# Kernel tuning notes

Hardware: AMD Instinct MI355X
Metric: run time of the kernel (lower is better)

Reference implementation:

```python
import jax, jax.numpy as jnp
import numpy as np

B, F, R, C = 16384, 256, 32, 16
H1, H2 = 128, 32        # FS-MLP hidden sizes
G1, G2 = 256, 64        # consequent MLP hidden sizes


def setup_inputs() -> dict:
    key = jax.random.key(0)
    ks = jax.random.split(key, 16)
    s = 0.05
    return {
        "data": jax.random.normal(ks[0], (B, F), jnp.float32),
        # per-rule antecedent params (torch inits proto=0, var=1; randomize proto for a nontrivial test)
        "proto": jax.random.normal(ks[1], (R, F), jnp.float32) * 0.1,
        "var": jnp.full((R, F), 0.05, jnp.float32),
        # shared FS-MLP: Linear(F,128)->ReLU->Linear(128,32)->ReLU->Linear(32,1)->ReLU
        "Wf1": jax.random.normal(ks[2], (H1, F), jnp.float32) * s,
        "bf1": jax.random.normal(ks[3], (H1,), jnp.float32) * s,
        "Wf2": jax.random.normal(ks[4], (H2, H1), jnp.float32) * s,
        "bf2": jax.random.normal(ks[5], (H2,), jnp.float32) * s,
        "Wf3": jax.random.normal(ks[6], (1, H2), jnp.float32) * s,
        "bf3": jax.random.normal(ks[7], (1,), jnp.float32) * s,
        # per-rule consequent MLP (stacked over rule dim): Linear(F,256)->ELU->Linear(256,64)->ELU->Linear(64,C)
        "Wc1": jax.random.normal(ks[8], (R, G1, F), jnp.float32) * s,
        "bc1": jax.random.normal(ks[9], (R, G1), jnp.float32) * s,
        "Wc2": jax.random.normal(ks[10], (R, G2, G1), jnp.float32) * s,
        "bc2": jax.random.normal(ks[11], (R, G2), jnp.float32) * s,
        "Wc3": jax.random.normal(ks[12], (R, C, G2), jnp.float32) * s,
        "bc3": jax.random.normal(ks[13], (R, C), jnp.float32) * s,
    }


def reference(data, proto, var, Wf1, bf1, Wf2, bf2, Wf3, bf3,
              Wc1, bc1, Wc2, bc2, Wc3, bc3):
    # Antecedent: Gaussian membership per rule -> [R, B, F]
    v = jnp.clip(var, 1e-4, 0.1)
    mem = jnp.exp(-(data[None, :, :] - proto[:, None, :]) ** 2
                  / (2.0 * v[:, None, :] ** 2))
    # Shared firing-strength MLP on each rule's membership tensor -> [R, B]
    h = jax.nn.relu(jnp.einsum('rbf,of->rbo', mem, Wf1) + bf1)
    h = jax.nn.relu(jnp.einsum('rbo,po->rbp', h, Wf2) + bf2)
    fs_ini = jax.nn.relu(jnp.einsum('rbp,qp->rbq', h, Wf3) + bf3)[..., 0]
    fire_strength = jax.nn.softmax(fs_ini.T, axis=1)  # [B, R], softmax over rules
    # Per-rule consequent MLPs on raw data (batched over rule dim) -> [R, B, C]
    c = jax.nn.elu(jnp.einsum('bf,rhf->rbh', data, Wc1) + bc1[:, None, :])
    c = jax.nn.elu(jnp.einsum('rbh,rgh->rbg', c, Wc2) + bc2[:, None, :])
    c = jax.nn.relu(jnp.einsum('rbg,rcg->rbc', c, Wc3) + bc3[:, None, :])
    # Softmax-weighted sum over rules -> [B, C]
    outputs = jnp.einsum('rbc,br->bc', c, fire_strength)
    return outputs, fire_strength
```

## Files before the change

### kernel.cpp

```cpp
#include <hip/hip_runtime.h>
#include <hip/hip_bf16.h>

#define BN 16384
#define FN 256
#define RN 32
#define CN 16
#define H1N 128
#define H2N 32
#define G1N 256
#define G2N 64

typedef __bf16 bf16_t;
typedef __bf16 bf16x8 __attribute__((ext_vector_type(8)));
typedef __bf16 bf16x4 __attribute__((ext_vector_type(4)));
typedef float f32x4 __attribute__((ext_vector_type(4)));

#define OFF_DATA   0UL
#define OFF_WF1    8388608UL
#define OFF_WF2    8454144UL
#define OFF_WC1    8462336UL
#define OFF_WC2    12656640UL
#define OFF_WC3    13705216UL
#define OFF_FSINI  13770752UL
#define OFF_C3     15867904UL

__device__ __forceinline__ f32x4 mfma16(bf16x8 a, bf16x8 b, f32x4 c) {
  return __builtin_amdgcn_mfma_f32_16x16x32_bf16(a, b, c, 0, 0, 0);
}

__device__ __forceinline__ float elu_f(float v) {
  float e = __builtin_amdgcn_exp2f(v * 1.44269504f) - 1.0f;
  return v > 0.f ? v : e;
}

__device__ __forceinline__ bf16x8 lfrag(const char* base, int strideB, int n0, int k0, int lane) {
  int row = n0 + (lane & 15);
  int off = (k0 * 2 + ((lane >> 4) << 4)) ^ ((row & 7) << 4);
  return *(const bf16x8*)(base + row * strideB + off);
}

__device__ __forceinline__ void pack_frag8(const float* __restrict__ src, bf16_t* __restrict__ dst,
                                           int NT, int KS, int g) {
  int per = NT * KS * 64;
  int r = g / per;
  int local = g - r * per;
  int lane = local & 63;
  int fr = local >> 6;
  int ks = fr / NT;
  int nt = fr - ks * NT;
  int N = NT * 16, K = KS * 32;
  int n = nt * 16 + (lane & 15);
  int k = ks * 32 + ((lane >> 4) << 3);
  const float* s = src + (long)r * N * K + (long)n * K + k;
  float4 a = *(const float4*)s;
  float4 b = *(const float4*)(s + 4);
  bf16x8 o;
  o[0] = (bf16_t)a.x; o[1] = (bf16_t)a.y; o[2] = (bf16_t)a.z; o[3] = (bf16_t)a.w;
  o[4] = (bf16_t)b.x; o[5] = (bf16_t)b.y; o[6] = (bf16_t)b.z; o[7] = (bf16_t)b.w;
  *(bf16x8*)(dst + (long)g * 8) = o;
}

#define G_DATA 524288
#define G_WC1  262144
#define G_WC2  65536
#define G_WF1  4096
#define G_WC3  4096
#define G_WF2  512
#define G_TOTAL (G_DATA + G_WC1 + G_WC2 + G_WF1 + G_WC3 + G_WF2)

__global__ __launch_bounds__(256) void k0_pack(
    const float* __restrict__ data, const float* __restrict__ Wf1, const float* __restrict__ Wf2,
    const float* __restrict__ Wc1, const float* __restrict__ Wc2, const float* __restrict__ Wc3,
    char* __restrict__ ws)
{
  int g = blockIdx.x * 256 + threadIdx.x;
  if (g < G_DATA) {
    const float* s = data + (long)g * 8;
    float4 a = *(const float4*)s, b = *(const float4*)(s + 4);
    bf16x8 o;
    o[0] = (bf16_t)a.x; o[1] = (bf16_t)a.y; o[2] = (bf16_t)a.z; o[3] = (bf16_t)a.w;
    o[4] = (bf16_t)b.x; o[5] = (bf16_t)b.y; o[6] = (bf16_t)b.z; o[7] = (bf16_t)b.w;
    *(bf16x8*)((bf16_t*)(ws + OFF_DATA) + (long)g * 8) = o;
    return;
  }
  g -= G_DATA;
  if (g < G_WC1) { pack_frag8(Wc1, (bf16_t*)(ws + OFF_WC1), 16, 8, g); return; }
  g -= G_WC1;
  if (g < G_WC2) { pack_frag8(Wc2, (bf16_t*)(ws + OFF_WC2), 4, 8, g); return; }
  g -= G_WC2;
  if (g < G_WF1) { pack_frag8(Wf1, (bf16_t*)(ws + OFF_WF1), 8, 8, g); return; }
  g -= G_WF1;
  if (g < G_WC3) { pack_frag8(Wc3, (bf16_t*)(ws + OFF_WC3), 1, 2, g); return; }
  g -= G_WF2 + G_WC3 - G_WC3;
  if (g < G_WC3) { }
  g -= 0;
  {
    if (g >= G_WC3) { g -= G_WC3; }
    if (g < G_WF2) { pack_frag8(Wf2, (bf16_t*)(ws + OFF_WF2), 2, 4, g); return; }
  }
}

__global__ __launch_bounds__(512, 4) void k1_fs(
    const float* __restrict__ data, const float* __restrict__ proto, const float* __restrict__ var,
    const float* __restrict__ bf1g, const float* __restrict__ bf2g,
    const float* __restrict__ Wf3g, const float* __restrict__ bf3g,
    const bf16_t* __restrict__ Wf1p, const bf16_t* __restrict__ Wf2p,
    float* __restrict__ fsini)
{
  __shared__ float proto_s[FN];
  __shared__ float ivar_s[FN];
  __shared__ __attribute__((aligned(16))) char mem_lds[128 * 512];

  const int r   = blockIdx.x >> 7;
  const int b0  = (blockIdx.x & 127) << 7;
  const int tid = threadIdx.x;
  const int lane = tid & 63;
  const int w   = tid >> 6;

  if (tid < FN) {
    proto_s[tid] = proto[r * FN + tid];
    float v = var[r * FN + tid];
    v = fminf(fmaxf(v, 1e-4f), 0.1f);
    ivar_s[tid] = 1.4426950408889634f * 0.5f / (v * v);
  }
  __syncthreads();

  {
    const int row = tid >> 2;
    const int f0  = (tid & 3) << 6;
    const float* dp = data + (long)(b0 + row) * FN + f0;
    char* mrow = mem_lds + row * 512;
    const int sw = (row & 7) << 4;
    #pragma unroll
    for (int i = 0; i < 8; ++i) {
      const int f = f0 + i * 8;
      float4 x0 = *(const float4*)(dp + i * 8);
      float4 x1 = *(const float4*)(dp + i * 8 + 4);
      bf16x8 m; float d;
      d = x0.x - proto_s[f + 0]; m[0] = (bf16_t)__builtin_amdgcn_exp2f(-d * d * ivar_s[f + 0]);
      d = x0.y - proto_s[f + 1]; m[1] = (bf16_t)__builtin_amdgcn_exp2f(-d * d * ivar_s[f + 1]);
      d = x0.z - proto_s[f + 2]; m[2] = (bf16_t)__builtin_amdgcn_exp2f(-d * d * ivar_s[f + 2]);
      d = x0.w - proto_s[f + 3]; m[3] = (bf16_t)__builtin_amdgcn_exp2f(-d * d * ivar_s[f + 3]);
      d = x1.x - proto_s[f + 4]; m[4] = (bf16_t)__builtin_amdgcn_exp2f(-d * d * ivar_s[f + 4]);
      d = x1.y - proto_s[f + 5]; m[5] = (bf16_t)__builtin_amdgcn_exp2f(-d * d * ivar_s[f + 5]);
      d = x1.z - proto_s[f + 6]; m[6] = (bf16_t)__builtin_amdgcn_exp2f(-d * d * ivar_s[f + 6]);
      d = x1.w - proto_s[f + 7]; m[7] = (bf16_t)__builtin_amdgcn_exp2f(-d * d * ivar_s[f + 7]);
      *(bf16x8*)(mrow + ((f * 2) ^ sw)) = m;
    }
  }
  __syncthreads();

  const int wm = w >> 2;
  const int wn = w & 3;
  f32x4 acc[4][2] = {};
  #pragma unroll
  for (int ks = 0; ks < 8; ++ks) {
    bf16x8 a[4], bb[2];
    #pragma unroll
    for (int i = 0; i < 4; ++i)
      a[i] = *(const bf16x8*)(Wf1p + (((ks * 8 + wm * 4 + i) * 64 + lane)) * 8);
    #pragma unroll
    for (int j = 0; j < 2; ++j)
      bb[j] = lfrag(mem_lds, 512, wn * 32 + j * 16, ks * 32, lane);
    #pragma unroll
    for (int i = 0; i < 4; ++i)
      #pragma unroll
      for (int j = 0; j < 2; ++j)
        acc[i][j] = mfma16(a[i], bb[j], acc[i][j]);
  }
  __syncthreads();

  #pragma unroll
  for (int i = 0; i < 4; ++i) {
    const int hb = wm * 64 + i * 16 + ((lane >> 4) << 2);
    f32x4 bias = *(const f32x4*)(bf1g + hb);
    #pragma unroll
    for (int j = 0; j < 2; ++j) {
      const int b = wn * 32 + j * 16 + (lane & 15);
      bf16x4 o;
      #pragma unroll
      for (int q = 0; q < 4; ++q)
        o[q] = (bf16_t)fmaxf(acc[i][j][q] + bias[q], 0.f);
      *(bf16x4*)(mem_lds + b * 256 + ((hb * 2) ^ ((b & 7) << 4))) = o;
    }
  }
  __syncthreads();

  float* h2s = (float*)(mem_lds + 32768);
  const int mt = w >> 2;
  f32x4 acc2[2] = {};
  #pragma unroll
  for (int ks = 0; ks < 4; ++ks) {
    bf16x8 a = *(const bf16x8*)(Wf2p + (((ks * 2 + mt) * 64 + lane)) * 8);
    #pragma unroll
    for (int j = 0; j < 2; ++j) {
      bf16x8 bb = lfrag(mem_lds, 256, (w & 3) * 32 + j * 16, ks * 32, lane);
      acc2[j] = mfma16(a, bb, acc2[j]);
    }
  }
  {
    const int p0 = mt * 16 + ((lane >> 4) << 2);
    f32x4 bias = *(const f32x4*)(bf2g + p0);
    #pragma unroll
    for (int j = 0; j < 2; ++j) {
      const int b = (w & 3) * 32 + j * 16 + (lane & 15);
      f32x4 o;
      #pragma unroll
      for (int q = 0; q < 4; ++q) o[q] = fmaxf(acc2[j][q] + bias[q], 0.f);
      *(f32x4*)(h2s + b * 40 + p0) = o;
    }
  }
  __syncthreads();

  if (tid < 128) {
    float s = bf3g[0];
    const float* hrow = h2s + tid * 40;
    #pragma unroll
    for (int p = 0; p < H2N; ++p) s += hrow[p] * Wf3g[p];
    fsini[(long)(b0 + tid) * RN + r] = fmaxf(s, 0.f);
  }
}

__global__ __launch_bounds__(256) void k2_softmax(const float* __restrict__ fsini,
                                                  float* __restrict__ fire)
{
  int b = blockIdx.x * 256 + threadIdx.x;
  float v[RN];
  const float4* p = (const float4*)(fsini + (long)b * RN);
  #pragma unroll
  for (int i = 0; i < RN / 4; ++i) {
    float4 t = p[i];
    v[4 * i] = t.x; v[4 * i + 1] = t.y; v[4 * i + 2] = t.z; v[4 * i + 3] = t.w;
  }
  float m = v[0];
  #pragma unroll
  for (int i = 1; i < RN; ++i) m = fmaxf(m, v[i]);
  float s = 0.f;
  #pragma unroll
  for (int i = 0; i < RN; ++i) { v[i] = expf(v[i] - m); s += v[i]; }
  float inv = 1.f / s;
  float4* o = (float4*)(fire + (long)b * RN);
  #pragma unroll
  for (int i = 0; i < RN / 4; ++i) {
    float4 t; t.x = v[4 * i] * inv; t.y = v[4 * i + 1] * inv;
    t.z = v[4 * i + 2] * inv; t.w = v[4 * i + 3] * inv;
    o[i] = t;
  }
}

__global__ __launch_bounds__(512, 4) void k3_cons(
    const bf16_t* __restrict__ datab,
    const bf16_t* __restrict__ Wc1p, const bf16_t* __restrict__ Wc2p, const bf16_t* __restrict__ Wc3p,
    const float* __restrict__ bc1, const float* __restrict__ bc2, const float* __restrict__ bc3,
    float* __restrict__ c3buf)
{
  __shared__ __attribute__((aligned(16))) char a_lds[128 * 512];
  __shared__ __attribute__((aligned(16))) char c2_lds[128 * 128];

  const int r   = blockIdx.x >> 7;
  const int b0  = (blockIdx.x & 127) << 7;
  const int tid = threadIdx.x;
  const int lane = tid & 63;
  const int w   = tid >> 6;

  {
    const int row = tid >> 2;
    const int e0  = (tid & 3) << 6;
    const bf16_t* sp = datab + (long)(b0 + row) * FN + e0;
    char* drow = a_lds + row * 512;
    const int sw = (row & 7) << 4;
    #pragma unroll
    for (int i = 0; i < 8; ++i) {
      bf16x8 v = *(const bf16x8*)(sp + i * 8);
      *(bf16x8*)(drow + (((e0 + i * 8) * 2) ^ sw)) = v;
    }
  }
  __syncthreads();

  const int wm = w >> 1;
  const int wn = w & 1;
  const bf16_t* W1 = Wc1p + (long)r * G1N * FN;
  f32x4 acc[4][4] = {};
  #pragma unroll
  for (int ks = 0; ks < 8; ++ks) {
    bf16x8 a[4], bb[4];
    #pragma unroll
    for (int i = 0; i < 4; ++i)
      a[i] = *(const bf16x8*)(W1 + (((ks * 16 + wm * 4 + i) * 64 + lane)) * 8);
    #pragma unroll
    for (int j = 0; j < 4; ++j)
      bb[j] = lfrag(a_lds, 512, wn * 64 + j * 16, ks * 32, lane);
    #pragma unroll
    for (int i = 0; i < 4; ++i)
      #pragma unroll
      for (int j = 0; j < 4; ++j)
        acc[i][j] = mfma16(a[i], bb[j], acc[i][j]);
  }
  __syncthreads();

  #pragma unroll
  for (int i = 0; i < 4; ++i) {
    const int g1b = wm * 64 + i * 16 + ((lane >> 4) << 2);
    f32x4 bias = *(const f32x4*)(bc1 + r * G1N + g1b);
    #pragma unroll
    for (int j = 0; j < 4; ++j) {
      const int b = wn * 64 + j * 16 + (lane & 15);
      bf16x4 o;
      #pragma unroll
      for (int q = 0; q < 4; ++q)
        o[q] = (bf16_t)elu_f(acc[i][j][q] + bias[q]);
      *(bf16x4*)(a_lds + b * 512 + ((g1b * 2) ^ ((b & 7) << 4))) = o;
    }
  }
  __syncthreads();

  const int wm2 = w >> 2;
  const int wn2 = w & 3;
  const bf16_t* W2 = Wc2p + (long)r * G2N * G1N;
  f32x4 acc2[2][2] = {};
  #pragma unroll
  for (int ks = 0; ks < 8; ++ks) {
    bf16x8 a[2], bb[2];
    #pragma unroll
    for (int i = 0; i < 2; ++i)
      a[i] = *(const bf16x8*)(W2 + (((ks * 4 + wm2 * 2 + i) * 64 + lane)) * 8);
    #pragma unroll
    for (int j = 0; j < 2; ++j)
      bb[j] = lfrag(a_lds, 512, wn2 * 32 + j * 16, ks * 32, lane);
    #pragma unroll
    for (int i = 0; i < 2; ++i)
      #pragma unroll
      for (int j = 0; j < 2; ++j)
        acc2[i][j] = mfma16(a[i], bb[j], acc2[i][j]);
  }
  #pragma unroll
  for (int i = 0; i < 2; ++i) {
    const int g2b = wm2 * 32 + i * 16 + ((lane >> 4) << 2);
    f32x4 bias = *(const f32x4*)(bc2 + r * G2N + g2b);
    #pragma unroll
    for (int j = 0; j < 2; ++j) {
      const int b = wn2 * 32 + j * 16 + (lane & 15);
      bf16x4 o;
      #pragma unroll
      for (int q = 0; q < 4; ++q)
        o[q] = (bf16_t)elu_f(acc2[i][j][q] + bias[q]);
      *(bf16x4*)(c2_lds + b * 128 + ((g2b * 2) ^ ((b & 7) << 4))) = o;
    }
  }
  __syncthreads();

  const bf16_t* W3 = Wc3p + (long)r * CN * G2N;
  f32x4 acc3 = {};
  #pragma unroll
  for (int ks = 0; ks < 2; ++ks) {
    bf16x8 a = *(const bf16x8*)(W3 + (((long)ks * 64 + lane)) * 8);
    bf16x8 bb = lfrag(c2_lds, 128, w * 16, ks * 32, lane);
    acc3 = mfma16(a, bb, acc3);
  }
  {
    const int c0 = ((lane >> 4) << 2);
    const int b  = w * 16 + (lane & 15);
    f32x4 bias = *(const f32x4*)(bc3 + r * CN + c0);
    f32x4 o;
    #pragma unroll
    for (int q = 0; q < 4; ++q) o[q] = fmaxf(acc3[q] + bias[q], 0.f);
    *(f32x4*)(c3buf + ((long)r * BN + b0 + b) * CN + c0) = o;
  }
}

__global__ __launch_bounds__(256) void k4_out(const float* __restrict__ c3buf,
                                              const float* __restrict__ fire,
                                              float* __restrict__ out)
{
  int t = blockIdx.x * 256 + threadIdx.x;
  int b = t >> 2, c4 = (t & 3) << 2;
  const float* fp = fire + (long)b * RN;
  f32x4 s = {};
  #pragma unroll
  for (int rr = 0; rr < RN; ++rr) {
    float fw = fp[rr];
    f32x4 v = *(const f32x4*)(c3buf + ((long)rr * BN + b) * CN + c4);
    s += fw * v;
  }
  *(f32x4*)(out + (long)b * CN + c4) = s;
}

extern "C" void kernel_launch(void* const* d_in, const int* in_sizes, int n_in,
                              void* d_out, int out_size, void* d_ws, size_t ws_size,
                              hipStream_t stream) {
  const float* data = (const float*)d_in[0];
  const float* proto = (const float*)d_in[1];
  const float* var  = (const float*)d_in[2];
  const float* Wf1  = (const float*)d_in[3];
  const float* bf1  = (const float*)d_in[4];
  const float* Wf2  = (const float*)d_in[5];
  const float* bf2  = (const float*)d_in[6];
  const float* Wf3  = (const float*)d_in[7];
  const float* bf3  = (const float*)d_in[8];
  const float* Wc1  = (const float*)d_in[9];
  const float* bc1  = (const float*)d_in[10];
  const float* Wc2  = (const float*)d_in[11];
  const float* bc2  = (const float*)d_in[12];
  const float* Wc3  = (const float*)d_in[13];
  const float* bc3  = (const float*)d_in[14];

  char* ws = (char*)d_ws;
  bf16_t* datab = (bf16_t*)(ws + OFF_DATA);
  bf16_t* Wf1p  = (bf16_t*)(ws + OFF_WF1);
  bf16_t* Wf2p  = (bf16_t*)(ws + OFF_WF2);
  bf16_t* Wc1p  = (bf16_t*)(ws + OFF_WC1);
  bf16_t* Wc2p  = (bf16_t*)(ws + OFF_WC2);
  bf16_t* Wc3p  = (bf16_t*)(ws + OFF_WC3);
  float*  fsini = (float*)(ws + OFF_FSINI);
  float*  c3buf = (float*)(ws + OFF_C3);

  float* out  = (float*)d_out;
  float* fire = out + (long)BN * CN;

  k0_pack<<<G_TOTAL / 256, 256, 0, stream>>>(data, Wf1, Wf2, Wc1, Wc2, Wc3, ws);
  k1_fs<<<RN * (BN / 128), 512, 0, stream>>>(data, proto, var, bf1, bf2, Wf3, bf3,
                                             Wf1p, Wf2p, fsini);
  k2_softmax<<<BN / 256, 256, 0, stream>>>(fsini, fire);
  k3_cons<<<RN * (BN / 128), 512, 0, stream>>>(datab, Wc1p, Wc2p, Wc3p, bc1, bc2, bc3, c3buf);
  k4_out<<<(BN * CN / 4) / 256, 256, 0, stream>>>(c3buf, fire, out);
}
```

Baseline: 264.9 us.

## Halve batch tile to 64 rows and remap blocks to rules per XCD

Both the firing-strength and consequent kernels now process 64 batch rows per block instead of 128. This halves LDS use and accumulator registers and doubles the grid, and the min-blocks hint is dropped from launch bounds. The consequent kernel maps block IDs so each XCD handles a contiguous group of four rules, aiming to keep each rule's weights in that XCD's L2. The trade-off is more blocks, each reloading the per-rule weights with less reuse across batch rows, and only half the waves active in the final layer.

```diff
diff --git a/kernel.cpp b/kernel.cpp
--- a/kernel.cpp
+++ b/kernel.cpp
@@ -91,16 +91,11 @@
   if (g < G_WF1) { pack_frag8(Wf1, (bf16_t*)(ws + OFF_WF1), 8, 8, g); return; }
   g -= G_WF1;
   if (g < G_WC3) { pack_frag8(Wc3, (bf16_t*)(ws + OFF_WC3), 1, 2, g); return; }
-  g -= G_WF2 + G_WC3 - G_WC3;
-  if (g < G_WC3) { }
-  g -= 0;
-  {
-    if (g >= G_WC3) { g -= G_WC3; }
-    if (g < G_WF2) { pack_frag8(Wf2, (bf16_t*)(ws + OFF_WF2), 2, 4, g); return; }
-  }
-}
-
-__global__ __launch_bounds__(512, 4) void k1_fs(
+  g -= G_WC3;
+  if (g < G_WF2) { pack_frag8(Wf2, (bf16_t*)(ws + OFF_WF2), 2, 4, g); return; }
+}
+
+__global__ __launch_bounds__(512) void k1_fs(
     const float* __restrict__ data, const float* __restrict__ proto, const float* __restrict__ var,
     const float* __restrict__ bf1g, const float* __restrict__ bf2g,
     const float* __restrict__ Wf3g, const float* __restrict__ bf3g,
@@ -109,10 +104,10 @@
 {
   __shared__ float proto_s[FN];
   __shared__ float ivar_s[FN];
-  __shared__ __attribute__((aligned(16))) char mem_lds[128 * 512];
-
-  const int r   = blockIdx.x >> 7;
-  const int b0  = (blockIdx.x & 127) << 7;
+  __shared__ __attribute__((aligned(16))) char fs_lds[36864];
+
+  const int r   = blockIdx.x >> 8;
+  const int b0  = (blockIdx.x & 255) << 6;
   const int tid = threadIdx.x;
   const int lane = tid & 63;
   const int w   = tid >> 6;
@@ -126,13 +121,13 @@
   __syncthreads();
 
   {
-    const int row = tid >> 2;
-    const int f0  = (tid & 3) << 6;
+    const int row = tid >> 3;
+    const int f0  = (tid & 7) << 5;
     const float* dp = data + (long)(b0 + row) * FN + f0;
-    char* mrow = mem_lds + row * 512;
+    char* mrow = fs_lds + row * 512;
     const int sw = (row & 7) << 4;
     #pragma unroll
-    for (int i = 0; i < 8; ++i) {
+    for (int i = 0; i < 4; ++i) {
       const int f = f0 + i * 8;
       float4 x0 = *(const float4*)(dp + i * 8);
       float4 x1 = *(const float4*)(dp + i * 8 + 4);
@@ -150,20 +145,20 @@
   }
   __syncthreads();
 
-  const int wm = w >> 2;
-  const int wn = w & 3;
-  f32x4 acc[4][2] = {};
+  const int mg = w >> 1;
+  const int ng = w & 1;
+  f32x4 acc[2][2] = {};
   #pragma unroll
   for (int ks = 0; ks < 8; ++ks) {
-    bf16x8 a[4], bb[2];
-    #pragma unroll
-    for (int i = 0; i < 4; ++i)
-      a[i] = *(const bf16x8*)(Wf1p + (((ks * 8 + wm * 4 + i) * 64 + lane)) * 8);
+    bf16x8 a[2], bb[2];
+    #pragma unroll
+    for (int i = 0; i < 2; ++i)
+      a[i] = *(const bf16x8*)(Wf1p + (((ks * 8 + mg * 2 + i) * 64 + lane)) * 8);
     #pragma unroll
     for (int j = 0; j < 2; ++j)
-      bb[j] = lfrag(mem_lds, 512, wn * 32 + j * 16, ks * 32, lane);
-    #pragma unroll
-    for (int i = 0; i < 4; ++i)
+      bb[j] = lfrag(fs_lds, 512, (ng * 2 + j) * 16, ks * 32, lane);
+    #pragma unroll
+    for (int i = 0; i < 2; ++i)
       #pragma unroll
       for (int j = 0; j < 2; ++j)
         acc[i][j] = mfma16(a[i], bb[j], acc[i][j]);
@@ -171,52 +166,45 @@
   __syncthreads();
 
   #pragma unroll
-  for (int i = 0; i < 4; ++i) {
-    const int hb = wm * 64 + i * 16 + ((lane >> 4) << 2);
+  for (int i = 0; i < 2; ++i) {
+    const int hb = (mg * 2 + i) * 16 + ((lane >> 4) << 2);
     f32x4 bias = *(const f32x4*)(bf1g + hb);
     #pragma unroll
     for (int j = 0; j < 2; ++j) {
-      const int b = wn * 32 + j * 16 + (lane & 15);
+      const int b = (ng * 2 + j) * 16 + (lane & 15);
       bf16x4 o;
       #pragma unroll
       for (int q = 0; q < 4; ++q)
         o[q] = (bf16_t)fmaxf(acc[i][j][q] + bias[q], 0.f);
-      *(bf16x4*)(mem_lds + b * 256 + ((hb * 2) ^ ((b & 7) << 4))) = o;
-    }
-  }
-  __syncthreads();
-
-  float* h2s = (float*)(mem_lds + 32768);
-  const int mt = w >> 2;
-  f32x4 acc2[2] = {};
-  #pragma unroll
-  for (int ks = 0; ks < 4; ++ks) {
-    bf16x8 a = *(const bf16x8*)(Wf2p + (((ks * 2 + mt) * 64 + lane)) * 8);
-    #pragma unroll
-    for (int j = 0; j < 2; ++j) {
-      bf16x8 bb = lfrag(mem_lds, 256, (w & 3) * 32 + j * 16, ks * 32, lane);
-      acc2[j] = mfma16(a, bb, acc2[j]);
-    }
-  }
+      *(bf16x4*)(fs_lds + b * 256 + ((hb * 2) ^ ((b & 7) << 4))) = o;
+    }
+  }
+  __syncthreads();
+
+  bf16_t* h2t = (bf16_t*)(fs_lds + 32768);
   {
-    const int p0 = mt * 16 + ((lane >> 4) << 2);
+    const int m = w >> 2;
+    const int n = w & 3;
+    f32x4 acc2 = {};
+    #pragma unroll
+    for (int ks = 0; ks < 4; ++ks) {
+      bf16x8 a = *(const bf16x8*)(Wf2p + (((ks * 2 + m) * 64 + lane)) * 8);
+      bf16x8 bb = lfrag(fs_lds, 256, n * 16, ks * 32, lane);
+      acc2 = mfma16(a, bb, acc2);
+    }
+    const int p0 = m * 16 + ((lane >> 4) << 2);
+    const int b  = n * 16 + (lane & 15);
     f32x4 bias = *(const f32x4*)(bf2g + p0);
     #pragma unroll
-    for (int j = 0; j < 2; ++j) {
-      const int b = (w & 3) * 32 + j * 16 + (lane & 15);
-      f32x4 o;
-      #pragma unroll
-      for (int q = 0; q < 4; ++q) o[q] = fmaxf(acc2[j][q] + bias[q], 0.f);
-      *(f32x4*)(h2s + b * 40 + p0) = o;
-    }
-  }
-  __syncthreads();
-
-  if (tid < 128) {
+    for (int q = 0; q < 4; ++q)
+      h2t[(p0 + q) * 64 + b] = (bf16_t)fmaxf(acc2[q] + bias[q], 0.f);
+  }
+  __syncthreads();
+
+  if (tid < 64) {
     float s = bf3g[0];
-    const float* hrow = h2s + tid * 40;
-    #pragma unroll
-    for (int p = 0; p < H2N; ++p) s += hrow[p] * Wf3g[p];
+    #pragma unroll
+    for (int p = 0; p < H2N; ++p) s += (float)h2t[p * 64 + tid] * Wf3g[p];
     fsini[(long)(b0 + tid) * RN + r] = fmaxf(s, 0.f);
   }
 }
@@ -248,29 +236,33 @@
   }
 }
 
-__global__ __launch_bounds__(512, 4) void k3_cons(
+__global__ __launch_bounds__(512) void k3_cons(
     const bf16_t* __restrict__ datab,
     const bf16_t* __restrict__ Wc1p, const bf16_t* __restrict__ Wc2p, const bf16_t* __restrict__ Wc3p,
     const float* __restrict__ bc1, const float* __restrict__ bc2, const float* __restrict__ bc3,
     float* __restrict__ c3buf)
 {
-  __shared__ __attribute__((aligned(16))) char a_lds[128 * 512];
-  __shared__ __attribute__((aligned(16))) char c2_lds[128 * 128];
-
-  const int r   = blockIdx.x >> 7;
-  const int b0  = (blockIdx.x & 127) << 7;
+  __shared__ __attribute__((aligned(16))) char a_lds[64 * 512];
+  __shared__ __attribute__((aligned(16))) char c2_lds[64 * 128];
+
+  const int bid = blockIdx.x;
+  const int xcd = bid & 7;
+  const int kk  = bid >> 3;
+  const int r   = xcd * 4 + (kk >> 8);
+  const int b0  = (kk & 255) << 6;
+
   const int tid = threadIdx.x;
   const int lane = tid & 63;
   const int w   = tid >> 6;
 
   {
-    const int row = tid >> 2;
-    const int e0  = (tid & 3) << 6;
+    const int row = tid >> 3;
+    const int e0  = (tid & 7) << 5;
     const bf16_t* sp = datab + (long)(b0 + row) * FN + e0;
     char* drow = a_lds + row * 512;
     const int sw = (row & 7) << 4;
     #pragma unroll
-    for (int i = 0; i < 8; ++i) {
+    for (int i = 0; i < 4; ++i) {
       bf16x8 v = *(const bf16x8*)(sp + i * 8);
       *(bf16x8*)(drow + (((e0 + i * 8) * 2) ^ sw)) = v;
     }
@@ -280,31 +272,31 @@
   const int wm = w >> 1;
   const int wn = w & 1;
   const bf16_t* W1 = Wc1p + (long)r * G1N * FN;
-  f32x4 acc[4][4] = {};
+  f32x4 acc[4][2] = {};
   #pragma unroll
   for (int ks = 0; ks < 8; ++ks) {
-    bf16x8 a[4], bb[4];
+    bf16x8 a[4], bb[2];
     #pragma unroll
     for (int i = 0; i < 4; ++i)
       a[i] = *(const bf16x8*)(W1 + (((ks * 16 + wm * 4 + i) * 64 + lane)) * 8);
     #pragma unroll
-    for (int j = 0; j < 4; ++j)
-      bb[j] = lfrag(a_lds, 512, wn * 64 + j * 16, ks * 32, lane);
+    for (int j = 0; j < 2; ++j)
+      bb[j] = lfrag(a_lds, 512, (wn * 2 + j) * 16, ks * 32, lane);
     #pragma unroll
     for (int i = 0; i < 4; ++i)
       #pragma unroll
-      for (int j = 0; j < 4; ++j)
+      for (int j = 0; j < 2; ++j)
         acc[i][j] = mfma16(a[i], bb[j], acc[i][j]);
   }
   __syncthreads();
 
   #pragma unroll
   for (int i = 0; i < 4; ++i) {
-    const int g1b = wm * 64 + i * 16 + ((lane >> 4) << 2);
+    const int g1b = (wm * 4 + i) * 16 + ((lane >> 4) << 2);
     f32x4 bias = *(const f32x4*)(bc1 + r * G1N + g1b);
     #pragma unroll
-    for (int j = 0; j < 4; ++j) {
-      const int b = wn * 64 + j * 16 + (lane & 15);
+    for (int j = 0; j < 2; ++j) {
+      const int b = (wn * 2 + j) * 16 + (lane & 15);
       bf16x4 o;
       #pragma unroll
       for (int q = 0; q < 4; ++q)
@@ -314,50 +306,43 @@
   }
   __syncthreads();
 
-  const int wm2 = w >> 2;
-  const int wn2 = w & 3;
+  const int m2 = w >> 1;
+  const int n2 = w & 1;
   const bf16_t* W2 = Wc2p + (long)r * G2N * G1N;
-  f32x4 acc2[2][2] = {};
+  f32x4 acc2[2] = {};
   #pragma unroll
   for (int ks = 0; ks < 8; ++ks) {
-    bf16x8 a[2], bb[2];
-    #pragma unroll
-    for (int i = 0; i < 2; ++i)
-      a[i] = *(const bf16x8*)(W2 + (((ks * 4 + wm2 * 2 + i) * 64 + lane)) * 8);
-    #pragma unroll
-    for (int j = 0; j < 2; ++j)
-      bb[j] = lfrag(a_lds, 512, wn2 * 32 + j * 16, ks * 32, lane);
-    #pragma unroll
-    for (int i = 0; i < 2; ++i)
-      #pragma unroll
-      for (int j = 0; j < 2; ++j)
-        acc2[i][j] = mfma16(a[i], bb[j], acc2[i][j]);
-  }
-  #pragma unroll
-  for (int i = 0; i < 2; ++i) {
-    const int g2b = wm2 * 32 + i * 16 + ((lane >> 4) << 2);
+    bf16x8 a = *(const bf16x8*)(W2 + (((ks * 4 + m2) * 64 + lane)) * 8);
+    #pragma unroll
+    for (int j = 0; j < 2; ++j) {
+      bf16x8 bb = lfrag(a_lds, 512, (n2 * 2 + j) * 16, ks * 32, lane);
+      acc2[j] = mfma16(a, bb, acc2[j]);
+    }
+  }
+  {
+    const int g2b = m2 * 16 + ((lane >> 4) << 2);
     f32x4 bias = *(const f32x4*)(bc2 + r * G2N + g2b);
     #pragma unroll
     for (int j = 0; j < 2; ++j) {
-      const int b = wn2 * 32 + j * 16 + (lane & 15);
+      const int b = (n2 * 2 + j) * 16 + (lane & 15);
       bf16x4 o;
       #pragma unroll
       for (int q = 0; q < 4; ++q)
-        o[q] = (bf16_t)elu_f(acc2[i][j][q] + bias[q]);
+        o[q] = (bf16_t)elu_f(acc2[j][q] + bias[q]);
       *(bf16x4*)(c2_lds + b * 128 + ((g2b * 2) ^ ((b & 7) << 4))) = o;
     }
   }
   __syncthreads();
 
-  const bf16_t* W3 = Wc3p + (long)r * CN * G2N;
-  f32x4 acc3 = {};
-  #pragma unroll
-  for (int ks = 0; ks < 2; ++ks) {
-    bf16x8 a = *(const bf16x8*)(W3 + (((long)ks * 64 + lane)) * 8);
-    bf16x8 bb = lfrag(c2_lds, 128, w * 16, ks * 32, lane);
-    acc3 = mfma16(a, bb, acc3);
-  }
-  {
+  if (w < 4) {
+    const bf16_t* W3 = Wc3p + (long)r * CN * G2N;
+    f32x4 acc3 = {};
+    #pragma unroll
+    for (int ks = 0; ks < 2; ++ks) {
+      bf16x8 a = *(const bf16x8*)(W3 + (((long)ks * 64 + lane)) * 8);
+      bf16x8 bb = lfrag(c2_lds, 128, w * 16, ks * 32, lane);
+      acc3 = mfma16(a, bb, acc3);
+    }
     const int c0 = ((lane >> 4) << 2);
     const int b  = w * 16 + (lane & 15);
     f32x4 bias = *(const f32x4*)(bc3 + r * CN + c0);
@@ -418,9 +403,9 @@
   float* fire = out + (long)BN * CN;
 
   k0_pack<<<G_TOTAL / 256, 256, 0, stream>>>(data, Wf1, Wf2, Wc1, Wc2, Wc3, ws);
-  k1_fs<<<RN * (BN / 128), 512, 0, stream>>>(data, proto, var, bf1, bf2, Wf3, bf3,
-                                             Wf1p, Wf2p, fsini);
+  k1_fs<<<RN * (BN / 64), 512, 0, stream>>>(data, proto, var, bf1, bf2, Wf3, bf3,
+                                            Wf1p, Wf2p, fsini);
   k2_softmax<<<BN / 256, 256, 0, stream>>>(fsini, fire);
-  k3_cons<<<RN * (BN / 128), 512, 0, stream>>>(datab, Wc1p, Wc2p, Wc3p, bc1, bc2, bc3, c3buf);
+  k3_cons<<<RN * (BN / 64), 512, 0, stream>>>(datab, Wc1p, Wc2p, Wc3p, bc1, bc2, bc3, c3buf);
   k4_out<<<(BN * CN / 4) / 256, 256, 0, stream>>>(c3buf, fire, out);
 }
```

Result: faster. 255.1 us (-3.7%).
